# Kernel tuning notes

Hardware: AMD Instinct MI355X
Metric: run time of the kernel (lower is better)

## Reference

```python
import jax, jax.numpy as jnp
import numpy as np

N = 50000
E = 400000
C_IN = 32
H = 64
RATIO = 0.5
SEQ_LEN = 5


def setup_inputs() -> dict:
    key = jax.random.key(0)
    ks = jax.random.split(key, 12)
    x = jax.random.normal(ks[0], (N, C_IN), jnp.float32)
    row = jax.random.randint(ks[1], (E,), 0, N, jnp.int32)
    off = jax.random.randint(ks[2], (E,), 1, N, jnp.int32)
    col = ((row + off) % N).astype(jnp.int32)  # no self-loops
    edge_index = jnp.stack([row, col])
    mask = jax.random.uniform(ks[3], (N,)) < 0.5

    def g(k, shape, fan):
        return jax.random.normal(k, shape, jnp.float32) / np.float32(np.sqrt(fan))

    return {
        "x": x, "edge_index": edge_index, "mask": mask,
        "conv0_w": g(ks[4], (C_IN, H), C_IN), "conv0_b": jnp.zeros((H,), jnp.float32),
        "conv1_w": g(ks[5], (H, H), H), "conv1_b": jnp.zeros((H,), jnp.float32),
        "pool_w": g(ks[6], (H,), H),
        "up_w": g(ks[7], (H, H), H), "up_b": jnp.zeros((H,), jnp.float32),
        "lstm0_w_ih": g(ks[8], (4 * H, H), H), "lstm0_w_hh": g(ks[9], (4 * H, H), H),
        "lstm0_b_ih": jnp.zeros((4 * H,), jnp.float32), "lstm0_b_hh": jnp.zeros((4 * H,), jnp.float32),
        "fin_w_ih": g(ks[10], (4 * H, H), H), "fin_w_hh": g(ks[11], (4 * H, H), H),
        "fin_b_ih": jnp.zeros((4 * H,), jnp.float32), "fin_b_hh": jnp.zeros((4 * H,), jnp.float32),
    }


def _coalesce(row, col, w, n):
    # sum duplicate (row, col) entries; output sorted by (row, col)
    key = row.astype(np.int64) * n + col.astype(np.int64)
    uk, inv = np.unique(key, return_inverse=True)
    w2 = np.bincount(inv, weights=w.astype(np.float64), minlength=uk.shape[0]).astype(np.float32)
    return uk // n, uk % n, w2


def _augment_adj(row, col, w, n):
    # remove self loops, add self loops (weight 1), compute A @ A (sparse), remove self loops
    m = row != col
    row = np.concatenate([row[m].astype(np.int64), np.arange(n, dtype=np.int64)])
    col = np.concatenate([col[m].astype(np.int64), np.arange(n, dtype=np.int64)])
    w = np.concatenate([w[m].astype(np.float32), np.ones(n, np.float32)])
    row, col, w = _coalesce(row, col, w, n)  # CSR-ordered
    cnt = np.bincount(row, minlength=n)
    indptr = np.concatenate([[0], np.cumsum(cnt)])
    dk = cnt[col]                      # out-degree of middle node k for each edge (i,k)
    starts = indptr[col]
    total = int(dk.sum())
    seg = np.repeat(np.cumsum(dk) - dk, dk)
    gi = np.repeat(starts, dk) + (np.arange(total) - seg)
    oi = np.repeat(row, dk)
    oj = col[gi]
    ow = np.repeat(w, dk) * w[gi]
    r2, c2, w2 = _coalesce(oi, oj, ow, n)
    m2 = r2 != c2
    return r2[m2], c2[m2], w2[m2]


def _gcn(x, row, col, ew, n, W, b):
    # GCNConv(improved=True): self-loop weight 2.0, symmetric deg^-1/2 normalization,
    # aggregate messages at target (col)
    h = x @ W
    loop = jnp.arange(n, dtype=row.dtype)
    r = jnp.concatenate([row, loop])
    c = jnp.concatenate([col, loop])
    w = jnp.concatenate([ew, jnp.full((n,), 2.0, ew.dtype)])
    deg = jax.ops.segment_sum(w, c, num_segments=n)
    dinv = jnp.where(deg > 0, jax.lax.rsqrt(deg), 0.0)
    norm = dinv[r] * w * dinv[c]
    out = jax.ops.segment_sum(norm[:, None] * h[r], c, num_segments=n)
    return out + b


def _sequences(x, mi):
    # sliding window [idx-L+1, idx] per masked node, zero left-padded
    t = mi[:, None] + jnp.arange(SEQ_LEN)[None, :] - (SEQ_LEN - 1)  # [M, L]
    return jnp.where((t >= 0)[:, :, None], x[jnp.clip(t, 0)], 0.0)


def _lstm_last(seq, w_ih, w_hh, b_ih, b_hh):
    # torch LSTM gate order: i, f, g, o; zero init state; return last hidden
    h = jnp.zeros((seq.shape[0], w_hh.shape[1]), seq.dtype)
    c = jnp.zeros_like(h)
    def step(carry, xt):
        h, c = carry
        g = xt @ w_ih.T + h @ w_hh.T + b_ih + b_hh
        i, f, gg, o = jnp.split(g, 4, axis=-1)
        c = jax.nn.sigmoid(f) * c + jax.nn.sigmoid(i) * jnp.tanh(gg)
        h = jax.nn.sigmoid(o) * jnp.tanh(c)
        return (h, c), None
    (h, _), _ = jax.lax.scan(step, (h, c), jnp.swapaxes(seq, 0, 1))
    return h


def reference(x, edge_index, mask, conv0_w, conv0_b, conv1_w, conv1_b, pool_w,
              up_w, up_b, lstm0_w_ih, lstm0_w_hh, lstm0_b_ih, lstm0_b_hh,
              fin_w_ih, fin_w_hh, fin_b_ih, fin_b_hh):
    n = x.shape[0]
    row0, col0 = edge_index[0], edge_index[1]
    ew0 = jnp.ones((row0.shape[0],), x.dtype)

    # down conv 0
    x1 = jax.nn.relu(_gcn(x, row0, col0, ew0, n, conv0_w, conv0_b))

    # augment_adj: sparse (A+I)^2 without diagonal (structural, constant)
    r2, c2, w2 = _augment_adj(np.asarray(row0), np.asarray(col0),
                              np.ones(row0.shape[0], np.float32), n)

    # TopKPooling: score = tanh((x.w)/||w||), keep top ceil(ratio*n)
    score = jnp.tanh((x1 @ pool_w) / jnp.linalg.norm(pool_w))
    k = int(np.ceil(RATIO * n))
    perm = np.argsort(-np.asarray(score), kind="stable")[:k]
    remap = np.full(n, -1, np.int64)
    remap[perm] = np.arange(k)
    keep = (remap[r2] >= 0) & (remap[c2] >= 0)
    pr = jnp.asarray(remap[r2[keep]].astype(np.int32))
    pc = jnp.asarray(remap[c2[keep]].astype(np.int32))
    pw = jnp.asarray(w2[keep])
    permj = jnp.asarray(perm.astype(np.int32))
    xp = x1[permj] * score[permj][:, None]

    # down conv 1 on pooled graph
    x2 = jax.nn.relu(_gcn(xp, pr, pc, pw, k, conv1_w, conv1_b))

    # up path (depth=1): LSTM over skip features at masked nodes
    mi = jnp.asarray(np.where(np.asarray(mask))[0].astype(np.int32))
    h0 = _lstm_last(_sequences(x1, mi), lstm0_w_ih, lstm0_w_hh, lstm0_b_ih, lstm0_b_hh)
    res = x1.at[mi].set(h0)
    up = jnp.zeros_like(x1).at[permj].set(x2)
    xo = _gcn(res + up, row0, col0, ew0, n, up_w, up_b)  # last level: no activation

    # final LSTM on masked nodes
    hf = _lstm_last(_sequences(xo, mi), fin_w_ih, fin_w_hh, fin_b_ih, fin_b_hh)
    return xo.at[mi].set(hf)
```

## Files before the change

### kernel.cpp

```cpp
#include <hip/hip_runtime.h>
#include <math.h>

#define NN 50000
#define EE 400000
#define CINV 32
#define KKEEP 25000
#define SEQL 5
#define HASH_BITS 20
#define HASH_SIZE (1u<<HASH_BITS)
#define HASH_MASK (HASH_SIZE-1u)
#define HEMPTY 0xFFFFFFFFu
#define PSB 196

typedef float vf4 __attribute__((ext_vector_type(4)));

__device__ __forceinline__ float sigm(float x){ return 1.f/(1.f+__expf(-x)); }

__global__ void k_init(uint2* __restrict__ hash, unsigned* __restrict__ hist,
                       int* __restrict__ degcnt, int* __restrict__ diagint,
                       int* __restrict__ ts, int* __restrict__ cs,
                       int* __restrict__ fillc, int* __restrict__ minv,
                       unsigned* scal, unsigned long long* selp,
                       const float* __restrict__ w0, const float* __restrict__ b0i,
                       const float* __restrict__ b0h, const float* __restrict__ wf,
                       const float* __restrict__ bfi, const float* __restrict__ bfh,
                       float* __restrict__ WT0, float* __restrict__ WTf,
                       float* __restrict__ bs0, float* __restrict__ bsf){
  int i = blockIdx.x*256 + threadIdx.x;
  if (i < (int)HASH_SIZE) hash[i] = make_uint2(HEMPTY, 0u);
  if (i < 4*65536) hist[i] = 0u;
  if (i < NN){ degcnt[i]=0; diagint[i]=0; ts[i]=0; cs[i]=0; fillc[i]=0; minv[i]=-1; }
  if (i < 256*64){
    int g = i>>6, k = i&63;
    WT0[k*256+g] = w0[i];
    WTf[k*256+g] = wf[i];
  }
  if (i < 256){ bs0[i]=b0i[i]+b0h[i]; bsf[i]=bfi[i]+bfh[i]; }
  if (i == 0){ scal[0]=0u; scal[1]=0u; scal[3]=KKEEP; selp[0]=0ull; }
}

__global__ void k_phase2(const int* __restrict__ row, const int* __restrict__ col,
                         const int* __restrict__ mp, int* __restrict__ degcnt,
                         uint2* __restrict__ tab, unsigned* scal){
  int e = blockIdx.x*256 + threadIdx.x;
  if (e < EE){
    int c = col[e];
    atomicAdd(&degcnt[c], 1);
    unsigned key = (unsigned)row[e]*50000u + (unsigned)c;
    unsigned h = (key*2654435761u) >> (32-HASH_BITS);
    for(;;){
      unsigned old = atomicCAS(&tab[h].x, HEMPTY, key);
      if (old==HEMPTY || old==key){ atomicAdd(&tab[h].y, 1u); break; }
      h = (h+1)&HASH_MASK;
    }
  }
  if (e < NN/4){ if ((unsigned)mp[e] > 1u) atomicOr(&scal[1], 1u); }
}

__global__ void k_psum1(const int* __restrict__ deg, int* __restrict__ part,
                        int* __restrict__ bsum, float* __restrict__ dinv){
  __shared__ int sc[256];
  int b = blockIdx.x, t = threadIdx.x, i = b*256+t;
  int v = (i<NN) ? deg[i] : 0;
  if (i < NN) dinv[i] = rsqrtf((float)v + 2.0f);
  sc[t] = v; __syncthreads();
  for (int o=1;o<256;o<<=1){
    int x = (t>=o) ? sc[t-o] : 0;
    __syncthreads();
    sc[t] += x;
    __syncthreads();
  }
  if (i < NN) part[i] = sc[t]-v;
  if (t == 255) bsum[b] = sc[255];
}
__global__ void k_psum2(const int* __restrict__ bsum, int* __restrict__ boff){
  __shared__ int sc[256];
  int t = threadIdx.x;
  int v = (t<PSB) ? bsum[t] : 0;
  sc[t] = v; __syncthreads();
  for (int o=1;o<256;o<<=1){
    int x = (t>=o) ? sc[t-o] : 0;
    __syncthreads();
    sc[t] += x;
    __syncthreads();
  }
  if (t < PSB) boff[t] = sc[t]-v;
}
__global__ void k_psum3(const int* __restrict__ part, const int* __restrict__ boff,
                        int* __restrict__ indptr){
  int i = blockIdx.x*256 + threadIdx.x;
  if (i < NN) indptr[i] = part[i] + boff[blockIdx.x];
  if (i == 0) indptr[NN] = EE;
}

__global__ void k_phase4(const int* __restrict__ row, const int* __restrict__ col,
                         const int* __restrict__ indptr, int* __restrict__ fillc,
                         int* __restrict__ csr_r, const uint2* __restrict__ tab,
                         int* __restrict__ diagint, const void* __restrict__ mp,
                         unsigned* scal, int* __restrict__ mlist, int* __restrict__ minv){
  int idx = blockIdx.x*256 + threadIdx.x;
  if (idx < EE){
    int r = row[idx], c = col[idx];
    int pos = indptr[c] + atomicAdd(&fillc[c], 1);
    csr_r[pos] = r;
    unsigned rkey = (unsigned)c*50000u + (unsigned)r;
    unsigned h = (rkey*2654435761u) >> (32-HASH_BITS);
    for(;;){
      unsigned kk = tab[h].x;
      if (kk==rkey){ atomicAdd(&diagint[r], (int)tab[h].y); break; }
      if (kk==HEMPTY) break;
      h = (h+1)&HASH_MASK;
    }
  } else {
    int i = idx - EE;
    if (i < NN){
      int mv = scal[1] ? (int)((const unsigned char*)mp)[i] : ((const int*)mp)[i];
      if (mv){ int p = (int)atomicAdd(&scal[0], 1u); mlist[p] = i; minv[i] = p; }
    }
  }
}

__global__ void k_mm_h0v(const float* __restrict__ X, const float* __restrict__ W, float* __restrict__ Y){
  int idx = blockIdx.x*256 + threadIdx.x;
  if (idx >= NN*16) return;
  int i = idx>>4, fq = idx&15;
  const vf4* X4 = (const vf4*)&X[i*CINV];
  const vf4* W4 = (const vf4*)W;
  vf4 acc = {0.f,0.f,0.f,0.f};
  #pragma unroll
  for (int kq=0;kq<CINV/4;kq++){
    vf4 xv = X4[kq];
    #pragma unroll
    for (int u=0;u<4;u++) acc += xv[u] * W4[(kq*4+u)*16+fq];
  }
  ((vf4*)Y)[i*16+fq] = acc;
}
__global__ void k_mm64v(const float* __restrict__ X, const float* __restrict__ W, float* __restrict__ Y){
  int idx = blockIdx.x*256 + threadIdx.x;
  if (idx >= NN*16) return;
  int i = idx>>4, fq = idx&15;
  const vf4* X4 = (const vf4*)&X[i*64];
  const vf4* W4 = (const vf4*)W;
  vf4 acc = {0.f,0.f,0.f,0.f};
  #pragma unroll
  for (int kq=0;kq<16;kq++){
    vf4 xv = X4[kq];
    #pragma unroll
    for (int u=0;u<4;u++) acc += xv[u] * W4[(kq*4+u)*16+fq];
  }
  ((vf4*)Y)[i*16+fq] = acc;
}
__global__ void k_mm64sv(const float* __restrict__ X, const float* __restrict__ W,
                         const float* __restrict__ sc, const int* __restrict__ kp,
                         float* __restrict__ Y){
  int idx = blockIdx.x*256 + threadIdx.x;
  if (idx >= NN*16) return;
  int i = idx>>4, fq = idx&15;
  if (!kp[i]) return;
  const vf4* X4 = (const vf4*)&X[i*64];
  const vf4* W4 = (const vf4*)W;
  vf4 acc = {0.f,0.f,0.f,0.f};
  #pragma unroll
  for (int kq=0;kq<16;kq++){
    vf4 xv = X4[kq];
    #pragma unroll
    for (int u=0;u<4;u++) acc += xv[u] * W4[(kq*4+u)*16+fq];
  }
  float s = sc[i];
  acc *= s;
  ((vf4*)Y)[i*16+fq] = acc;
}

__global__ void g_gcn0(const int* __restrict__ indptr, const int* __restrict__ csr_r,
                       const float* __restrict__ dinv, const float* __restrict__ H,
                       const float* __restrict__ b, const float* __restrict__ pw,
                       float* __restrict__ out, unsigned long long* __restrict__ keys,
                       float* __restrict__ score){
  int node = blockIdx.x*4 + (threadIdx.x>>6), lane = threadIdx.x&63;
  if (node >= NN) return;
  int s = __builtin_amdgcn_readfirstlane(indptr[node]);
  int e = __builtin_amdgcn_readfirstlane(indptr[node+1]);
  float acc = 0.f;
  for (int j=s;j<e;j++){
    int r = __builtin_amdgcn_readfirstlane(csr_r[j]);
    acc += dinv[r]*H[r*64+lane];
  }
  float di = dinv[node];
  float v = di*acc + 2.f*di*di*H[node*64+lane] + b[lane];
  float x1v = fmaxf(v, 0.f);
  out[node*64+lane] = x1v;
  float pv = pw[lane];
  float nq = pv*pv;
  float dq = x1v*pv;
  for (int o=32;o;o>>=1){ nq += __shfl_down(nq, o, 64); dq += __shfl_down(dq, o, 64); }
  if (lane==0){
    float sv = tanhf(dq / sqrtf(nq));
    sv = sv + 0.0f;
    score[node] = sv;
    unsigned u = __float_as_uint(sv);
    unsigned asc = (u>>31) ? ~u : (u | 0x80000000u);
    keys[node] = (((unsigned long long)(~asc))<<32) | (unsigned)node;
  }
}
__global__ void g_t2(const int* __restrict__ indptr, const int* __restrict__ csr_r,
                     const float* __restrict__ dinv1, const float* __restrict__ hp,
                     float* __restrict__ t2){
  int node = blockIdx.x*4 + (threadIdx.x>>6), lane = threadIdx.x&63;
  if (node >= NN) return;
  int s = __builtin_amdgcn_readfirstlane(indptr[node]);
  int e = __builtin_amdgcn_readfirstlane(indptr[node+1]);
  float acc = dinv1[node]*hp[node*64+lane];
  for (int j=s;j<e;j++){
    int r = __builtin_amdgcn_readfirstlane(csr_r[j]);
    float dr = dinv1[r];
    if (dr != 0.f) acc += dr*hp[r*64+lane];
  }
  t2[node*64+lane] = acc;
}
__global__ void g_agg2y(const int* __restrict__ indptr, const int* __restrict__ csr_r,
                        const float* __restrict__ t2, const float* __restrict__ hp,
                        const float* __restrict__ dinv1, const int* __restrict__ diagint,
                        const int* __restrict__ kp, const float* __restrict__ b1,
                        const float* __restrict__ C, const float* __restrict__ Hbuf,
                        const int* __restrict__ minv, float* __restrict__ D){
  int node = blockIdx.x*4 + (threadIdx.x>>6), lane = threadIdx.x&63;
  if (node >= NN) return;
  int mv = minv[node];
  float base = (mv >= 0) ? Hbuf[(size_t)mv*64+lane] : C[node*64+lane];
  float add = 0.f;
  if (kp[node]){
    int s = __builtin_amdgcn_readfirstlane(indptr[node]);
    int e = __builtin_amdgcn_readfirstlane(indptr[node+1]);
    float acc = t2[node*64+lane];
    for (int j=s;j<e;j++){
      int r = __builtin_amdgcn_readfirstlane(csr_r[j]);
      acc += t2[r*64+lane];
    }
    float di = dinv1[node], hv = hp[node*64+lane];
    float diag = (float)(diagint[node] + 1);
    float v = di*(acc - diag*di*hv) + 2.f*di*di*hv + b1[lane];
    add = fmaxf(v, 0.f);
  }
  D[node*64+lane] = base + add;
}
__global__ void g_up(const int* __restrict__ indptr, const int* __restrict__ csr_r,
                     const float* __restrict__ dinv, const float* __restrict__ H,
                     const float* __restrict__ b, float* __restrict__ xo, float* __restrict__ out){
  int node = blockIdx.x*4 + (threadIdx.x>>6), lane = threadIdx.x&63;
  if (node >= NN) return;
  int s = __builtin_amdgcn_readfirstlane(indptr[node]);
  int e = __builtin_amdgcn_readfirstlane(indptr[node+1]);
  float acc = 0.f;
  for (int j=s;j<e;j++){
    int r = __builtin_amdgcn_readfirstlane(csr_r[j]);
    acc += dinv[r]*H[r*64+lane];
  }
  float di = dinv[node];
  float v = di*acc + 2.f*di*di*H[node*64+lane] + b[lane];
  xo[node*64+lane] = v; out[node*64+lane] = v;
}

__global__ void k_hist(const unsigned long long* __restrict__ keys, unsigned* __restrict__ hist,
                       const unsigned long long* __restrict__ selp, int round){
  int i = blockIdx.x*256 + threadIdx.x;
  if (i >= NN) return;
  unsigned long long key = keys[i];
  int shift = 48 - 16*round;
  if (round==0 || (key>>(shift+16)) == selp[0])
    atomicAdd(&hist[(unsigned)((key>>shift)&0xFFFFull)], 1u);
}
__global__ void k_pick(const unsigned* __restrict__ hist, unsigned long long* selp, unsigned* scal){
  __shared__ unsigned csum[256];
  __shared__ unsigned bins[256];
  __shared__ int schunk;
  int t = threadIdx.x;
  const uint4* h4 = (const uint4*)(hist + t*256);
  unsigned s = 0;
  #pragma unroll 8
  for (int j=0;j<64;j++){ uint4 v = h4[j]; s += v.x+v.y+v.z+v.w; }
  csum[t] = s;
  __syncthreads();
  if (t==0){
    unsigned rem = scal[3];
    int chunk = 255;
    for (int c2=0;c2<256;c2++){ unsigned cc=csum[c2]; if (rem>cc) rem-=cc; else { chunk=c2; break; } }
    schunk = chunk; scal[3] = rem;
  }
  __syncthreads();
  bins[t] = hist[schunk*256 + t];
  __syncthreads();
  if (t==0){
    unsigned rem = scal[3];
    int bin = schunk*256 + 255;
    for (int b=0;b<256;b++){ unsigned hv=bins[b]; if (rem>hv) rem-=hv; else { bin = schunk*256 + b; break; } }
    selp[0] = (selp[0]<<16) | (unsigned long long)(unsigned)bin;
    scal[3] = rem;
  }
}
__global__ void k_mid(const int* __restrict__ row, const int* __restrict__ col,
                      const unsigned long long* __restrict__ keys,
                      const unsigned long long* __restrict__ selp,
                      int* __restrict__ kp, int* __restrict__ ts){
  int idx = blockIdx.x*256 + threadIdx.x;
  unsigned long long sp = selp[0];
  if (idx < EE){
    if (keys[row[idx]] <= sp) atomicAdd(&ts[col[idx]], 1);
  } else {
    int i = idx - EE;
    if (i < NN){
      int k = (keys[i] <= sp) ? 1 : 0;
      kp[i] = k;
      if (k) atomicAdd(&ts[i], 1);
    }
  }
}
__global__ void k_colsum(const int* __restrict__ row, const int* __restrict__ col,
                         const int* __restrict__ ts, int* __restrict__ cs){
  int idx = blockIdx.x*256 + threadIdx.x;
  if (idx < EE){ int v = ts[row[idx]]; if (v) atomicAdd(&cs[col[idx]], v); }
  else { int i = idx-EE; if (i < NN){ int v = ts[i]; if (v) atomicAdd(&cs[i], v); } }
}
__global__ void k_dinv1(const int* __restrict__ cs, const int* __restrict__ diagint,
                        const int* __restrict__ kp, float* __restrict__ dinv1){
  int i = blockIdx.x*256 + threadIdx.x;
  if (i >= NN) return;
  dinv1[i] = kp[i] ? rsqrtf((float)(cs[i] - diagint[i] - 1) + 2.0f) : 0.f;
}

__global__ __launch_bounds__(256) void k_xw(const float* __restrict__ src,
        const float* __restrict__ WT, const float* __restrict__ bsum,
        float* __restrict__ XW){
  __shared__ vf4 Wl[4096];
  int t = threadIdx.x;
  const vf4* Wg = (const vf4*)WT;
  for (int u=t; u<4096; u+=256) Wl[u] = Wg[u];
  int fq = t & 63, wv = t >> 6;
  vf4 bias = ((const vf4*)bsum)[fq];
  __syncthreads();
  for (int node = blockIdx.x*4 + wv; node < NN; node += gridDim.x*4){
    const vf4* X4 = (const vf4*)&src[(size_t)node*64];
    vf4 acc = bias;
    #pragma unroll 4
    for (int kq=0;kq<16;kq++){
      vf4 xv = X4[kq];
      acc += xv.x * Wl[(kq*4+0)*64+fq];
      acc += xv.y * Wl[(kq*4+1)*64+fq];
      acc += xv.z * Wl[(kq*4+2)*64+fq];
      acc += xv.w * Wl[(kq*4+3)*64+fq];
    }
    ((vf4*)XW)[(size_t)node*64+fq] = acc;
  }
}

__global__ __launch_bounds__(256) void k_rec(const float* __restrict__ XW,
        const float* __restrict__ whh, const float* __restrict__ bsum,
        const int* __restrict__ mlist, const unsigned* __restrict__ scal,
        float* __restrict__ dst, int scatter){
  int M = (int)scal[0];
  if (M < 0 || M > NN) M = 0;
  int w = threadIdx.x>>6, lane = threadIdx.x&63;
  int r = w*64 + lane;
  const vf4* g4 = (const vf4*)&whh[(size_t)r*64];
  vf4 wh[16];
  #pragma unroll
  for (int j=0;j<16;j++) wh[j] = g4[j];
  __shared__ float sh[4][64];
  __shared__ float gates[4][4][64];
  int ntask = (M+3)>>2;
  for (int task = blockIdx.x; task < ntask; task += gridDim.x){
    int m = task*4 + w;
    bool valid = (m < M);
    int node = mlist[valid ? m : (M-1)];
    float c, h;
    {
      int rowi = node - (SEQL-1);
      float g0,g1,g2,g3;
      if (rowi >= 0){
        const float* p = &XW[(size_t)rowi*256];
        g0=p[lane]; g1=p[64+lane]; g2=p[128+lane]; g3=p[192+lane];
      } else {
        g0=bsum[lane]; g1=bsum[64+lane]; g2=bsum[128+lane]; g3=bsum[192+lane];
      }
      c = sigm(g0)*tanhf(g2);
      h = sigm(g3)*tanhf(c);
      sh[w][lane] = h;
    }
    __syncthreads();
    for (int t=1;t<SEQL;t++){
      vf4 a0={0,0,0,0}, a1={0,0,0,0}, a2={0,0,0,0}, a3={0,0,0,0};
      #pragma unroll
      for (int j=0;j<16;j++){
        vf4 wj = wh[j];
        a0 += (*(const vf4*)&sh[0][j*4]) * wj;
        a1 += (*(const vf4*)&sh[1][j*4]) * wj;
        a2 += (*(const vf4*)&sh[2][j*4]) * wj;
        a3 += (*(const vf4*)&sh[3][j*4]) * wj;
      }
      gates[0][w][lane] = a0.x+a0.y+a0.z+a0.w;
      gates[1][w][lane] = a1.x+a1.y+a1.z+a1.w;
      gates[2][w][lane] = a2.x+a2.y+a2.z+a2.w;
      gates[3][w][lane] = a3.x+a3.y+a3.z+a3.w;
      __syncthreads();
      int rowi = node - (SEQL-1) + t;
      float x0,x1,x2,x3;
      if (rowi >= 0){
        const float* p = &XW[(size_t)rowi*256];
        x0=p[lane]; x1=p[64+lane]; x2=p[128+lane]; x3=p[192+lane];
      } else {
        x0=bsum[lane]; x1=bsum[64+lane]; x2=bsum[128+lane]; x3=bsum[192+lane];
      }
      float gi = gates[w][0][lane] + x0;
      float gf = gates[w][1][lane] + x1;
      float gg = gates[w][2][lane] + x2;
      float go = gates[w][3][lane] + x3;
      c = sigm(gf)*c + sigm(gi)*tanhf(gg);
      h = sigm(go)*tanhf(c);
      sh[w][lane] = h;
      __syncthreads();
    }
    if (valid){
      size_t o = scatter ? ((size_t)node*64 + lane) : ((size_t)m*64 + lane);
      dst[o] = h;
    }
  }
}

extern "C" void kernel_launch(void* const* d_in, const int* in_sizes, int n_in,
                              void* d_out, int out_size, void* d_ws, size_t ws_size,
                              hipStream_t stream) {
  const float* x   = (const float*)d_in[0];
  const int*   ei  = (const int*)d_in[1];
  const int*   row = ei;
  const int*   col = ei + EE;
  const void*  mp  = d_in[2];
  const float* W0  = (const float*)d_in[3];
  const float* b0  = (const float*)d_in[4];
  const float* W1  = (const float*)d_in[5];
  const float* b1  = (const float*)d_in[6];
  const float* pw  = (const float*)d_in[7];
  const float* Wu  = (const float*)d_in[8];
  const float* bu  = (const float*)d_in[9];
  const float* l0wih=(const float*)d_in[10];
  const float* l0whh=(const float*)d_in[11];
  const float* l0bih=(const float*)d_in[12];
  const float* l0bhh=(const float*)d_in[13];
  const float* lfwih=(const float*)d_in[14];
  const float* lfwhh=(const float*)d_in[15];
  const float* lfbih=(const float*)d_in[16];
  const float* lfbhh=(const float*)d_in[17];

  char* wp = (char*)d_ws;
  auto alloc = [&](size_t bytes)->char*{ char* p = wp; wp += ((bytes+255)/256)*256; return p; };
  float* A     = (float*)alloc((size_t)NN*64*4);
  float* B     = (float*)alloc((size_t)NN*64*4);
  float* C     = (float*)alloc((size_t)NN*64*4);
  float* D     = (float*)alloc((size_t)NN*64*4);
  float* Ebuf  = (float*)alloc((size_t)NN*64*4);
  float* Hbuf  = (float*)alloc((size_t)NN*64*4);
  float* XW    = (float*)alloc((size_t)NN*256*4);
  float* WT0   = (float*)alloc((size_t)256*64*4);
  float* WTf   = (float*)alloc((size_t)256*64*4);
  float* bs0   = (float*)alloc((size_t)256*4);
  float* bsf   = (float*)alloc((size_t)256*4);
  float* score = (float*)alloc((size_t)NN*4);
  float* dinv0 = (float*)alloc((size_t)NN*4);
  float* dinv1 = (float*)alloc((size_t)NN*4);
  unsigned long long* keys = (unsigned long long*)alloc((size_t)NN*8);
  int* degcnt  = (int*)alloc((size_t)NN*4);
  int* diagint = (int*)alloc((size_t)NN*4);
  int* ts      = (int*)alloc((size_t)NN*4);
  int* cs      = (int*)alloc((size_t)NN*4);
  int* kp      = (int*)alloc((size_t)NN*4);
  int* mlist   = (int*)alloc((size_t)NN*4);
  int* minv    = (int*)alloc((size_t)NN*4);
  int* indptr  = (int*)alloc((size_t)(NN+1)*4);
  int* part    = (int*)alloc((size_t)NN*4);
  int* fillc   = (int*)alloc((size_t)NN*4);
  int* bsum    = (int*)alloc((size_t)256*4);
  int* boff    = (int*)alloc((size_t)256*4);
  int* csr_r   = (int*)alloc((size_t)EE*4);
  uint2* hash  = (uint2*)alloc((size_t)HASH_SIZE*8);
  unsigned* hist=(unsigned*)alloc((size_t)4*65536*4);
  unsigned* scal=(unsigned*)alloc(256);
  unsigned long long* selp = (unsigned long long*)(scal + 4);

  #define GRID1(n) dim3(((n)+255)/256), dim3(256), 0, stream
  #define GRIDW dim3((NN+3)/4), dim3(256), 0, stream

  k_init<<<GRID1(HASH_SIZE)>>>(hash, hist, degcnt, diagint, ts, cs, fillc, minv,
                               scal, selp, l0wih, l0bih, l0bhh, lfwih, lfbih, lfbhh,
                               WT0, WTf, bs0, bsf);
  k_phase2<<<GRID1(EE)>>>(row, col, (const int*)mp, degcnt, hash, scal);
  k_psum1<<<dim3(PSB),dim3(256),0,stream>>>(degcnt, part, bsum, dinv0);
  k_psum2<<<dim3(1),dim3(256),0,stream>>>(bsum, boff);
  k_psum3<<<dim3(PSB),dim3(256),0,stream>>>(part, boff, indptr);
  k_phase4<<<GRID1(EE+NN)>>>(row, col, indptr, fillc, csr_r, hash, diagint, mp, scal, mlist, minv);

  k_mm_h0v<<<GRID1(NN*16)>>>(x, W0, A);
  g_gcn0<<<GRIDW>>>(indptr, csr_r, dinv0, A, b0, pw, C, keys, score);

  for (int r2=0;r2<4;r2++){
    k_hist<<<GRID1(NN)>>>(keys, hist + r2*65536, selp, r2);
    k_pick<<<dim3(1),dim3(256),0,stream>>>(hist + r2*65536, selp, scal);
  }
  k_mid<<<GRID1(EE+NN)>>>(row, col, keys, selp, kp, ts);
  k_colsum<<<GRID1(EE+NN)>>>(row, col, ts, cs);
  k_dinv1<<<GRID1(NN)>>>(cs, diagint, kp, dinv1);

  k_mm64sv<<<GRID1(NN*16)>>>(C, W1, score, kp, Ebuf);
  g_t2<<<GRIDW>>>(indptr, csr_r, dinv1, Ebuf, A);

  k_xw<<<dim3(512),dim3(256),0,stream>>>(C, WT0, bs0, XW);
  k_rec<<<dim3(1024),dim3(256),0,stream>>>(XW, l0whh, bs0, mlist, scal, Hbuf, 0);

  g_agg2y<<<GRIDW>>>(indptr, csr_r, A, Ebuf, dinv1, diagint, kp, b1, C, Hbuf, minv, D);

  k_mm64v<<<GRID1(NN*16)>>>(D, Wu, Ebuf);
  g_up<<<GRIDW>>>(indptr, csr_r, dinv0, Ebuf, bu, B, (float*)d_out);

  k_xw<<<dim3(512),dim3(256),0,stream>>>(B, WTf, bsf, XW);
  k_rec<<<dim3(1024),dim3(256),0,stream>>>(XW, lfwhh, bsf, mlist, scal, (float*)d_out, 1);
  #undef GRIDW
  #undef GRID1
}
```

Before: 770.0 us.

## Fuse first top-k histogram into GCN, use CSR gathers for pooled degrees, fast LSTM math

```diff
diff --git a/kernel.cpp b/kernel.cpp
--- a/kernel.cpp
+++ b/kernel.cpp
@@ -14,11 +14,11 @@
 
 typedef float vf4 __attribute__((ext_vector_type(4)));
 
-__device__ __forceinline__ float sigm(float x){ return 1.f/(1.f+__expf(-x)); }
+__device__ __forceinline__ float sigm(float x){ return __builtin_amdgcn_rcpf(1.f+__expf(-x)); }
+__device__ __forceinline__ float ftanh(float x){ return 1.f - 2.f*__builtin_amdgcn_rcpf(1.f+__expf(2.f*x)); }
 
 __global__ void k_init(uint2* __restrict__ hash, unsigned* __restrict__ hist,
                        int* __restrict__ degcnt, int* __restrict__ diagint,
-                       int* __restrict__ ts, int* __restrict__ cs,
                        int* __restrict__ fillc, int* __restrict__ minv,
                        unsigned* scal, unsigned long long* selp,
                        const float* __restrict__ w0, const float* __restrict__ b0i,
@@ -29,7 +29,7 @@
   int i = blockIdx.x*256 + threadIdx.x;
   if (i < (int)HASH_SIZE) hash[i] = make_uint2(HEMPTY, 0u);
   if (i < 4*65536) hist[i] = 0u;
-  if (i < NN){ degcnt[i]=0; diagint[i]=0; ts[i]=0; cs[i]=0; fillc[i]=0; minv[i]=-1; }
+  if (i < NN){ degcnt[i]=0; diagint[i]=0; fillc[i]=0; minv[i]=-1; }
   if (i < 256*64){
     int g = i>>6, k = i&63;
     WT0[k*256+g] = w0[i];
@@ -175,7 +175,7 @@
                        const float* __restrict__ dinv, const float* __restrict__ H,
                        const float* __restrict__ b, const float* __restrict__ pw,
                        float* __restrict__ out, unsigned long long* __restrict__ keys,
-                       float* __restrict__ score){
+                       float* __restrict__ score, unsigned* __restrict__ hist){
   int node = blockIdx.x*4 + (threadIdx.x>>6), lane = threadIdx.x&63;
   if (node >= NN) return;
   int s = __builtin_amdgcn_readfirstlane(indptr[node]);
@@ -199,7 +199,9 @@
     score[node] = sv;
     unsigned u = __float_as_uint(sv);
     unsigned asc = (u>>31) ? ~u : (u | 0x80000000u);
-    keys[node] = (((unsigned long long)(~asc))<<32) | (unsigned)node;
+    unsigned desc = ~asc;
+    keys[node] = (((unsigned long long)desc)<<32) | (unsigned)node;
+    atomicAdd(&hist[desc>>16], 1u);
   }
 }
 __global__ void g_t2(const int* __restrict__ indptr, const int* __restrict__ csr_r,
@@ -266,7 +268,7 @@
   if (i >= NN) return;
   unsigned long long key = keys[i];
   int shift = 48 - 16*round;
-  if (round==0 || (key>>(shift+16)) == selp[0])
+  if ((key>>(shift+16)) == selp[0])
     atomicAdd(&hist[(unsigned)((key>>shift)&0xFFFFull)], 1u);
 }
 __global__ void k_pick(const unsigned* __restrict__ hist, unsigned long long* selp, unsigned* scal){
@@ -297,34 +299,29 @@
     scal[3] = rem;
   }
 }
-__global__ void k_mid(const int* __restrict__ row, const int* __restrict__ col,
+__global__ void k_tsg(const int* __restrict__ indptr, const int* __restrict__ csr_r,
                       const unsigned long long* __restrict__ keys,
                       const unsigned long long* __restrict__ selp,
                       int* __restrict__ kp, int* __restrict__ ts){
-  int idx = blockIdx.x*256 + threadIdx.x;
-  unsigned long long sp = selp[0];
-  if (idx < EE){
-    if (keys[row[idx]] <= sp) atomicAdd(&ts[col[idx]], 1);
-  } else {
-    int i = idx - EE;
-    if (i < NN){
-      int k = (keys[i] <= sp) ? 1 : 0;
-      kp[i] = k;
-      if (k) atomicAdd(&ts[i], 1);
-    }
-  }
-}
-__global__ void k_colsum(const int* __restrict__ row, const int* __restrict__ col,
-                         const int* __restrict__ ts, int* __restrict__ cs){
-  int idx = blockIdx.x*256 + threadIdx.x;
-  if (idx < EE){ int v = ts[row[idx]]; if (v) atomicAdd(&cs[col[idx]], v); }
-  else { int i = idx-EE; if (i < NN){ int v = ts[i]; if (v) atomicAdd(&cs[i], v); } }
-}
-__global__ void k_dinv1(const int* __restrict__ cs, const int* __restrict__ diagint,
-                        const int* __restrict__ kp, float* __restrict__ dinv1){
   int i = blockIdx.x*256 + threadIdx.x;
   if (i >= NN) return;
-  dinv1[i] = kp[i] ? rsqrtf((float)(cs[i] - diagint[i] - 1) + 2.0f) : 0.f;
+  unsigned long long sp = selp[0];
+  int s = indptr[i], e = indptr[i+1];
+  int self = (keys[i] <= sp) ? 1 : 0;
+  kp[i] = self;
+  int acc = self;
+  for (int j=s;j<e;j++) acc += (keys[csr_r[j]] <= sp) ? 1 : 0;
+  ts[i] = acc;
+}
+__global__ void k_csg(const int* __restrict__ indptr, const int* __restrict__ csr_r,
+                      const int* __restrict__ ts, const int* __restrict__ diagint,
+                      const int* __restrict__ kp, float* __restrict__ dinv1){
+  int i = blockIdx.x*256 + threadIdx.x;
+  if (i >= NN) return;
+  int s = indptr[i], e = indptr[i+1];
+  int acc = ts[i];
+  for (int j=s;j<e;j++) acc += ts[csr_r[j]];
+  dinv1[i] = kp[i] ? rsqrtf((float)(acc - diagint[i] - 1) + 2.0f) : 0.f;
 }
 
 __global__ __launch_bounds__(256) void k_xw(const float* __restrict__ src,
@@ -371,22 +368,30 @@
     int m = task*4 + w;
     bool valid = (m < M);
     int node = mlist[valid ? m : (M-1)];
+    node = min(max(node, 0), NN-1);
     float c, h;
+    float x0,x1,x2,x3;
     {
       int rowi = node - (SEQL-1);
-      float g0,g1,g2,g3;
       if (rowi >= 0){
         const float* p = &XW[(size_t)rowi*256];
-        g0=p[lane]; g1=p[64+lane]; g2=p[128+lane]; g3=p[192+lane];
+        x0=p[lane]; x1=p[64+lane]; x2=p[128+lane]; x3=p[192+lane];
       } else {
-        g0=bsum[lane]; g1=bsum[64+lane]; g2=bsum[128+lane]; g3=bsum[192+lane];
+        x0=bsum[lane]; x1=bsum[64+lane]; x2=bsum[128+lane]; x3=bsum[192+lane];
       }
-      c = sigm(g0)*tanhf(g2);
-      h = sigm(g3)*tanhf(c);
+      c = sigm(x0)*ftanh(x2);
+      h = sigm(x3)*ftanh(c);
       sh[w][lane] = h;
     }
     __syncthreads();
     for (int t=1;t<SEQL;t++){
+      int rowi = node - (SEQL-1) + t;
+      if (rowi >= 0){
+        const float* p = &XW[(size_t)rowi*256];
+        x0=p[lane]; x1=p[64+lane]; x2=p[128+lane]; x3=p[192+lane];
+      } else {
+        x0=bsum[lane]; x1=bsum[64+lane]; x2=bsum[128+lane]; x3=bsum[192+lane];
+      }
       vf4 a0={0,0,0,0}, a1={0,0,0,0}, a2={0,0,0,0}, a3={0,0,0,0};
       #pragma unroll
       for (int j=0;j<16;j++){
@@ -401,20 +406,12 @@
       gates[2][w][lane] = a2.x+a2.y+a2.z+a2.w;
       gates[3][w][lane] = a3.x+a3.y+a3.z+a3.w;
       __syncthreads();
-      int rowi = node - (SEQL-1) + t;
-      float x0,x1,x2,x3;
-      if (rowi >= 0){
-        const float* p = &XW[(size_t)rowi*256];
-        x0=p[lane]; x1=p[64+lane]; x2=p[128+lane]; x3=p[192+lane];
-      } else {
-        x0=bsum[lane]; x1=bsum[64+lane]; x2=bsum[128+lane]; x3=bsum[192+lane];
-      }
       float gi = gates[w][0][lane] + x0;
       float gf = gates[w][1][lane] + x1;
       float gg = gates[w][2][lane] + x2;
       float go = gates[w][3][lane] + x3;
-      c = sigm(gf)*c + sigm(gi)*tanhf(gg);
-      h = sigm(go)*tanhf(c);
+      c = sigm(gf)*c + sigm(gi)*ftanh(gg);
+      h = sigm(go)*ftanh(c);
       sh[w][lane] = h;
       __syncthreads();
     }
@@ -469,7 +466,6 @@
   int* degcnt  = (int*)alloc((size_t)NN*4);
   int* diagint = (int*)alloc((size_t)NN*4);
   int* ts      = (int*)alloc((size_t)NN*4);
-  int* cs      = (int*)alloc((size_t)NN*4);
   int* kp      = (int*)alloc((size_t)NN*4);
   int* mlist   = (int*)alloc((size_t)NN*4);
   int* minv    = (int*)alloc((size_t)NN*4);
@@ -487,7 +483,7 @@
   #define GRID1(n) dim3(((n)+255)/256), dim3(256), 0, stream
   #define GRIDW dim3((NN+3)/4), dim3(256), 0, stream
 
-  k_init<<<GRID1(HASH_SIZE)>>>(hash, hist, degcnt, diagint, ts, cs, fillc, minv,
+  k_init<<<GRID1(HASH_SIZE)>>>(hash, hist, degcnt, diagint, fillc, minv,
                                scal, selp, l0wih, l0bih, l0bhh, lfwih, lfbih, lfbhh,
                                WT0, WTf, bs0, bsf);
   k_phase2<<<GRID1(EE)>>>(row, col, (const int*)mp, degcnt, hash, scal);
@@ -497,15 +493,15 @@
   k_phase4<<<GRID1(EE+NN)>>>(row, col, indptr, fillc, csr_r, hash, diagint, mp, scal, mlist, minv);
 
   k_mm_h0v<<<GRID1(NN*16)>>>(x, W0, A);
-  g_gcn0<<<GRIDW>>>(indptr, csr_r, dinv0, A, b0, pw, C, keys, score);
-
-  for (int r2=0;r2<4;r2++){
+  g_gcn0<<<GRIDW>>>(indptr, csr_r, dinv0, A, b0, pw, C, keys, score, hist);
+
+  k_pick<<<dim3(1),dim3(256),0,stream>>>(hist, selp, scal);
+  for (int r2=1;r2<4;r2++){
     k_hist<<<GRID1(NN)>>>(keys, hist + r2*65536, selp, r2);
     k_pick<<<dim3(1),dim3(256),0,stream>>>(hist + r2*65536, selp, scal);
   }
-  k_mid<<<GRID1(EE+NN)>>>(row, col, keys, selp, kp, ts);
-  k_colsum<<<GRID1(EE+NN)>>>(row, col, ts, cs);
-  k_dinv1<<<GRID1(NN)>>>(cs, diagint, kp, dinv1);
+  k_tsg<<<GRID1(NN)>>>(indptr, csr_r, keys, selp, kp, ts);
+  k_csg<<<GRID1(NN)>>>(indptr, csr_r, ts, diagint, kp, dinv1);
 
   k_mm64sv<<<GRID1(NN*16)>>>(C, W1, score, kp, Ebuf);
   g_t2<<<GRIDW>>>(indptr, csr_r, dinv1, Ebuf, A);
```

Measured after the change: 716.5 us. -6.9%, faster.
